# Kernel optimization log

Hardware: AMD Instinct MI355X
Metric: run time of the kernel (lower is better)

The kernel has to match this reference:

```python
import jax, jax.numpy as jnp
import numpy as np

N_GROUP = 8
TOPK_GROUP = 4
TOP_K = 8
ROUTED_SCALING = 2.5
NUM_EXPERTS = 256
HIDDEN = 7168
TOKENS = 8192


def setup_inputs() -> dict:
    key = jax.random.key(0)
    k1, k2, k3 = jax.random.split(key, 3)
    hidden_states = jax.random.normal(k1, (TOKENS, HIDDEN), dtype=jnp.float32)
    weight = jax.random.normal(k2, (NUM_EXPERTS, HIDDEN), dtype=jnp.float32) * 0.02
    e_score_correction_bias = jax.random.normal(k3, (NUM_EXPERTS,), dtype=jnp.float32) * 0.1
    return {"hidden_states": hidden_states, "weight": weight,
            "e_score_correction_bias": e_score_correction_bias}


def reference(hidden_states, weight, e_score_correction_bias):
    # logits = x @ W^T  (fp32 gate GEMM)
    logits = jnp.einsum('th,eh->te', hidden_states.astype(jnp.float32), weight)
    scores = jax.nn.sigmoid(logits)                       # [T, E]
    swb = scores + e_score_correction_bias                # [T, E]
    T, E = swb.shape
    gsize = E // N_GROUP
    # per-group score = sum of top-2 biased scores within each group
    grouped = swb.reshape(T, N_GROUP, gsize)
    top2, _ = jax.lax.top_k(grouped, 2)                   # [T, G, 2]
    group_scores = top2.sum(axis=-1)                      # [T, G]
    # keep topk_group groups
    _, gidx = jax.lax.top_k(group_scores, TOPK_GROUP)     # [T, topk_group]
    rows = jnp.arange(T)[:, None]
    group_mask = jnp.zeros((T, N_GROUP), jnp.float32).at[rows, gidx].set(1.0)
    score_mask = jnp.repeat(group_mask, gsize, axis=-1)   # [T, E]
    swb_masked = swb * score_mask
    # top_k experts among kept groups
    _, tidx = jax.lax.top_k(swb_masked, TOP_K)            # [T, top_k]
    new_mask = jnp.zeros((T, E), jnp.float32).at[rows, tidx].set(1.0)
    sel = scores * new_mask
    score_sum = sel.sum(axis=-1, keepdims=True) + 1e-20
    return sel / score_sum * ROUTED_SCALING
```

## Files before the change

### kernel.cpp

```cpp
#include <hip/hip_runtime.h>
#include <math.h>

#define TOKENS   8192
#define HIDDEN   7168
#define NEXPERT  256
#define NGROUP   8
#define TOPKG    4
#define TOPK     8
#define SCALE    2.5f

#define BM 128
#define BN 128
#define BK 32
#define KSPLIT 4
#define KPB (HIDDEN / KSPLIT)
#define NT  (KPB / BK)
#define WTILE_BYTES 32768

#define RSTR 72

typedef _Float16 half8 __attribute__((ext_vector_type(8)));
typedef _Float16 half4 __attribute__((ext_vector_type(4)));
typedef float    floatx4 __attribute__((ext_vector_type(4)));

__device__ __forceinline__ void cvt_store(_Float16* __restrict__ H,
                                          int row, int k0, float4 v) {
    half4 h, l;
    h[0] = (_Float16)v.x; h[1] = (_Float16)v.y;
    h[2] = (_Float16)v.z; h[3] = (_Float16)v.w;
    l[0] = (_Float16)(v.x - (float)h[0]);
    l[1] = (_Float16)(v.y - (float)h[1]);
    l[2] = (_Float16)(v.z - (float)h[2]);
    l[3] = (_Float16)(v.w - (float)h[3]);
    const int base = row * RSTR + ((k0 >> 3) << 4) + (k0 & 7);
    *(half4*)&H[base]     = h;
    *(half4*)&H[base + 8] = l;
}

__device__ __forceinline__ void cvt8(const float4 a, const float4 b,
                                     half8& h, half8& l) {
    h[0] = (_Float16)a.x; h[1] = (_Float16)a.y;
    h[2] = (_Float16)a.z; h[3] = (_Float16)a.w;
    h[4] = (_Float16)b.x; h[5] = (_Float16)b.y;
    h[6] = (_Float16)b.z; h[7] = (_Float16)b.w;
    l[0] = (_Float16)(a.x - (float)h[0]); l[1] = (_Float16)(a.y - (float)h[1]);
    l[2] = (_Float16)(a.z - (float)h[2]); l[3] = (_Float16)(a.w - (float)h[3]);
    l[4] = (_Float16)(b.x - (float)h[4]); l[5] = (_Float16)(b.y - (float)h[5]);
    l[6] = (_Float16)(b.z - (float)h[6]); l[7] = (_Float16)(b.w - (float)h[7]);
}

__global__ __launch_bounds__(896) void wsplit_kernel(
    const float* __restrict__ W, char* __restrict__ WS, float* __restrict__ O)
{
    const int gt = blockIdx.x * 896 + threadIdx.x;
#pragma unroll
    for (int i = 0; i < 3; i++) {
        const int idx = gt + i * (NEXPERT * 896);
        if (idx < TOKENS * NEXPERT / 4)
            *(float4*)&O[(size_t)idx * 4] = float4{0.f, 0.f, 0.f, 0.f};
    }

    const int e  = blockIdx.x;
    const int og = threadIdx.x;
    const float4 a = *(const float4*)&W[(size_t)e * HIDDEN + og * 8];
    const float4 b = *(const float4*)&W[(size_t)e * HIDDEN + og * 8 + 4];
    half8 h, l;
    cvt8(a, b, h, l);

    const int kz = og / (KPB / 8);
    const int tt = (og % (KPB / 8)) >> 2;
    const int oc = og & 3;
    char* p = WS + (size_t)(kz * NT + tt) * WTILE_BYTES + (e * 4 + oc) * 32;
    *(half8*)p        = h;
    *(half8*)(p + 16) = l;
}

__global__ __launch_bounds__(256, 2) void gate_gemm_kernel(
    const float* __restrict__ X, const char* __restrict__ WS,
    float* __restrict__ OUT)
{
    __shared__ _Float16 Ab[2][BM * RSTR];

    const int tid = threadIdx.x;
    const int nb  = blockIdx.x * BN;
    const int mb  = blockIdx.y * BM;
    const int kb  = blockIdx.z * KPB;

    const int srow = tid >> 3;
    const int sk0  = (tid & 7) * 4;
    const float* Aptr = X + (size_t)(mb + srow) * HIDDEN + kb + sk0;

    const int lane = tid & 63, wave = tid >> 6;
    const int wm = (wave >> 1) * 64, wn = (wave & 1) * 64;
    const int fr = lane & 15, quad = lane >> 4;

    const char* Bbase = WS + (size_t)(blockIdx.z * NT) * WTILE_BYTES
                      + (nb + wn + fr) * 128 + quad * 32;

    float4 av[4];
#pragma unroll
    for (int q = 0; q < 4; q++)
        av[q] = *(const float4*)(Aptr + (size_t)(q * 32) * HIDDEN);
    half8 bhA[4], blA[4], bhB[4], blB[4];
#pragma unroll
    for (int j = 0; j < 4; j++) {
        bhA[j] = *(const half8*)(Bbase + j * 2048);
        blA[j] = *(const half8*)(Bbase + j * 2048 + 16);
    }

    floatx4 acc[4][4];
#pragma unroll
    for (int i = 0; i < 4; i++)
#pragma unroll
        for (int j = 0; j < 4; j++) acc[i][j] = floatx4{0.f, 0.f, 0.f, 0.f};

#define STEP(T, BHC, BLC, BHN, BLN)                                           \
    {                                                                         \
        _Pragma("unroll")                                                     \
        for (int q = 0; q < 4; q++)                                           \
            cvt_store(Ab[(T) & 1], q * 32 + srow, sk0, av[q]);                \
        const int tn = ((T) + 1 < NT) ? (T) + 1 : NT - 1;                     \
        _Pragma("unroll")                                                     \
        for (int q = 0; q < 4; q++)                                           \
            av[q] = *(const float4*)(Aptr + tn * BK                           \
                                     + (size_t)(q * 32) * HIDDEN);            \
        __syncthreads();                                                      \
        const _Float16* Ac = Ab[(T) & 1];                                     \
        half8 ah[4], al[4];                                                   \
        _Pragma("unroll")                                                     \
        for (int i = 0; i < 4; i++) {                                         \
            const int a = (wm + i * 16 + fr) * RSTR + quad * 16;              \
            ah[i] = *(const half8*)&Ac[a];                                    \
            al[i] = *(const half8*)&Ac[a + 8];                                \
        }                                                                     \
        const char* bp = Bbase + (size_t)tn * WTILE_BYTES;                    \
        _Pragma("unroll")                                                     \
        for (int j = 0; j < 4; j++) {                                         \
            BHN[j] = *(const half8*)(bp + j * 2048);                          \
            BLN[j] = *(const half8*)(bp + j * 2048 + 16);                     \
        }                                                                     \
        _Pragma("unroll")                                                     \
        for (int j = 0; j < 4; j++)                                           \
            _Pragma("unroll")                                                 \
            for (int i = 0; i < 4; i++) {                                     \
                acc[i][j] = __builtin_amdgcn_mfma_f32_16x16x32_f16(           \
                    al[i], BHC[j], acc[i][j], 0, 0, 0);                       \
                acc[i][j] = __builtin_amdgcn_mfma_f32_16x16x32_f16(           \
                    ah[i], BLC[j], acc[i][j], 0, 0, 0);                       \
                acc[i][j] = __builtin_amdgcn_mfma_f32_16x16x32_f16(           \
                    ah[i], BHC[j], acc[i][j], 0, 0, 0);                       \
            }                                                                 \
    }

    for (int t = 0; t < NT; t += 2) {
        STEP(t,     bhA, blA, bhB, blB)
        STEP(t + 1, bhB, blB, bhA, blA)
    }
#undef STEP

#pragma unroll
    for (int i = 0; i < 4; i++)
#pragma unroll
        for (int j = 0; j < 4; j++) {
            const int col = nb + wn + j * 16 + fr;
#pragma unroll
            for (int r = 0; r < 4; r++) {
                const int row = mb + wm + i * 16 + quad * 4 + r;
                atomicAdd(&OUT[(size_t)row * NEXPERT + col], acc[i][j][r]);
            }
        }
}

__global__ __launch_bounds__(256) void route_kernel(
    float* __restrict__ S, const float* __restrict__ bias)
{
    const int lane = threadIdx.x & 63;
    const int wave = threadIdx.x >> 6;
    const int t    = blockIdx.x * 4 + wave;

    const float4 lg4 = *(const float4*)&S[(size_t)t * NEXPERT + lane * 4];
    const float4 b4  = *(const float4*)&bias[lane * 4];
    float sc[4];
    sc[0] = 1.0f / (1.0f + expf(-lg4.x));
    sc[1] = 1.0f / (1.0f + expf(-lg4.y));
    sc[2] = 1.0f / (1.0f + expf(-lg4.z));
    sc[3] = 1.0f / (1.0f + expf(-lg4.w));
    float swb[4] = { sc[0] + b4.x, sc[1] + b4.y, sc[2] + b4.z, sc[3] + b4.w };

    float m1 = -INFINITY, m2 = -INFINITY;
#pragma unroll
    for (int j = 0; j < 4; j++) {
        const float v = swb[j];
        if (v > m1)      { m2 = m1; m1 = v; }
        else if (v > m2) { m2 = v; }
    }
#pragma unroll
    for (int s = 1; s < 8; s <<= 1) {
        const float o1 = __shfl_xor(m1, s, 64);
        const float o2 = __shfl_xor(m2, s, 64);
        const float hi = fmaxf(m1, o1);
        const float lo = fminf(m1, o1);
        m2 = fmaxf(lo, fmaxf(m2, o2));
        m1 = hi;
    }
    const float gs = m1 + m2;

    float gsc[NGROUP];
#pragma unroll
    for (int g = 0; g < NGROUP; g++) gsc[g] = __shfl(gs, g * 8, 64);
    const int myg = lane >> 3;
    int rank = 0;
#pragma unroll
    for (int g = 0; g < NGROUP; g++)
        rank += (gsc[g] > gs) || (gsc[g] == gs && g < myg);
    const bool kept = (rank < TOPKG);

    float v[4];
#pragma unroll
    for (int j = 0; j < 4; j++) v[j] = kept ? swb[j] : 0.0f;

    float sum = 0.0f;
    int selmask = 0;
    for (int r = 0; r < TOPK; r++) {
        float bv = -INFINITY;
        int   bi = 0x7fffffff;
#pragma unroll
        for (int j = 0; j < 4; j++) {
            const bool avail = ((selmask >> j) & 1) == 0;
            if (avail && v[j] > bv) { bv = v[j]; bi = lane * 4 + j; }
        }
#pragma unroll
        for (int s = 1; s < 64; s <<= 1) {
            const float ov = __shfl_xor(bv, s, 64);
            const int   oi = __shfl_xor(bi, s, 64);
            if (ov > bv || (ov == bv && oi < bi)) { bv = ov; bi = oi; }
        }
        const int wl = bi >> 2, wj = bi & 3;
        const float mysc = (wj == 0) ? sc[0] : (wj == 1) ? sc[1]
                         : (wj == 2) ? sc[2] : sc[3];
        sum += __shfl(mysc, wl, 64);
        if (lane == wl) selmask |= (1 << wj);
    }

    const float rcp = SCALE / (sum + 1e-20f);
    float4 o;
    o.x = (selmask & 1) ? sc[0] * rcp : 0.0f;
    o.y = (selmask & 2) ? sc[1] * rcp : 0.0f;
    o.z = (selmask & 4) ? sc[2] * rcp : 0.0f;
    o.w = (selmask & 8) ? sc[3] * rcp : 0.0f;
    *(float4*)&S[(size_t)t * NEXPERT + lane * 4] = o;
}

extern "C" void kernel_launch(void* const* d_in, const int* in_sizes, int n_in,
                              void* d_out, int out_size, void* d_ws, size_t ws_size,
                              hipStream_t stream) {
    const float* X    = (const float*)d_in[0];
    const float* W    = (const float*)d_in[1];
    const float* bias = (const float*)d_in[2];
    float* out = (float*)d_out;
    char* ws = (char*)d_ws; (void)ws_size;

    wsplit_kernel<<<NEXPERT, 896, 0, stream>>>(W, ws, out);
    dim3 ggrid(NEXPERT / BN, TOKENS / BM, KSPLIT);
    gate_gemm_kernel<<<ggrid, 256, 0, stream>>>(X, ws, out);
    route_kernel<<<TOKENS / 4, 256, 0, stream>>>(out, bias);
}
```

Measured before the change: 434.3 us.

## Stage weight tiles through LDS and interleave MFMA with next-tile staging

Weights are re-laid out per 128-expert block so each GEMM block loads its B tile cooperatively into LDS, rather than each wave reading its own fragments straight from global memory. The main loop is restructured into a software pipeline: half the MFMAs run, then the next A/B tiles are converted and stored to LDS and the tile after that is prefetched, then the remaining MFMAs run, with one barrier per step. s_setprio and a sched_barrier are added to prioritise MFMA issue. The goal is less redundant global traffic for B and better overlap of loads with compute, at the cost of more LDS use (which may limit occupancy) and more registers for the double prefetch.

```diff
diff --git a/kernel.cpp b/kernel.cpp
--- a/kernel.cpp
+++ b/kernel.cpp
@@ -15,7 +15,7 @@
 #define KSPLIT 4
 #define KPB (HIDDEN / KSPLIT)
 #define NT  (KPB / BK)
-#define WTILE_BYTES 32768
+#define TILE_BYTES 16384
 
 #define RSTR 72
 
@@ -70,7 +70,9 @@
     const int kz = og / (KPB / 8);
     const int tt = (og % (KPB / 8)) >> 2;
     const int oc = og & 3;
-    char* p = WS + (size_t)(kz * NT + tt) * WTILE_BYTES + (e * 4 + oc) * 32;
+    const int row = e & 127, nb = e >> 7;
+    char* p = WS + (size_t)((nb * KSPLIT + kz) * NT + tt) * TILE_BYTES
+            + (row * 4 + oc) * 32;
     *(half8*)p        = h;
     *(half8*)(p + 16) = l;
 }
@@ -80,6 +82,7 @@
     float* __restrict__ OUT)
 {
     __shared__ _Float16 Ab[2][BM * RSTR];
+    __shared__ _Float16 Bb[2][BN * RSTR];
 
     const int tid = threadIdx.x;
     const int nb  = blockIdx.x * BN;
@@ -90,23 +93,47 @@
     const int sk0  = (tid & 7) * 4;
     const float* Aptr = X + (size_t)(mb + srow) * HIDDEN + kb + sk0;
 
+    const char* Wimg =
+        WS + (size_t)((blockIdx.x * KSPLIT + blockIdx.z) * NT) * TILE_BYTES;
+    const int bbase[2] = { (tid >> 2) * RSTR + (tid & 3) * 16,
+                           ((tid >> 2) + 64) * RSTR + (tid & 3) * 16 };
+
     const int lane = tid & 63, wave = tid >> 6;
     const int wm = (wave >> 1) * 64, wn = (wave & 1) * 64;
     const int fr = lane & 15, quad = lane >> 4;
 
-    const char* Bbase = WS + (size_t)(blockIdx.z * NT) * WTILE_BYTES
-                      + (nb + wn + fr) * 128 + quad * 32;
-
-    float4 av[4];
+    float4 avA[4], avB[4];
+    half8  nhA[2], nlA[2], nhB[2], nlB[2];
 #pragma unroll
     for (int q = 0; q < 4; q++)
-        av[q] = *(const float4*)(Aptr + (size_t)(q * 32) * HIDDEN);
-    half8 bhA[4], blA[4], bhB[4], blB[4];
-#pragma unroll
-    for (int j = 0; j < 4; j++) {
-        bhA[j] = *(const half8*)(Bbase + j * 2048);
-        blA[j] = *(const half8*)(Bbase + j * 2048 + 16);
-    }
+        avA[q] = *(const float4*)(Aptr + (size_t)(q * 32) * HIDDEN);
+#pragma unroll
+    for (int s = 0; s < 2; s++) {
+        const char* src = Wimg + (tid + 256 * s) * 32;
+        nhA[s] = *(const half8*)src;
+        nlA[s] = *(const half8*)(src + 16);
+    }
+#pragma unroll
+    for (int q = 0; q < 4; q++)
+        cvt_store(Ab[0], q * 32 + srow, sk0, avA[q]);
+#pragma unroll
+    for (int s = 0; s < 2; s++) {
+        *(half8*)&Bb[0][bbase[s]]     = nhA[s];
+        *(half8*)&Bb[0][bbase[s] + 8] = nlA[s];
+    }
+#pragma unroll
+    for (int q = 0; q < 4; q++)
+        avB[q] = *(const float4*)(Aptr + BK + (size_t)(q * 32) * HIDDEN);
+    {
+        const char* srcT = Wimg + (size_t)1 * TILE_BYTES;
+#pragma unroll
+        for (int s = 0; s < 2; s++) {
+            const char* src = srcT + (tid + 256 * s) * 32;
+            nhB[s] = *(const half8*)src;
+            nlB[s] = *(const half8*)(src + 16);
+        }
+    }
+    __syncthreads();
 
     floatx4 acc[4][4];
 #pragma unroll
@@ -114,47 +141,80 @@
 #pragma unroll
         for (int j = 0; j < 4; j++) acc[i][j] = floatx4{0.f, 0.f, 0.f, 0.f};
 
-#define STEP(T, BHC, BLC, BHN, BLN)                                           \
+#define STEP(T, AVC, NHC, NLC, AVN, NHN, NLN)                                 \
     {                                                                         \
-        _Pragma("unroll")                                                     \
-        for (int q = 0; q < 4; q++)                                           \
-            cvt_store(Ab[(T) & 1], q * 32 + srow, sk0, av[q]);                \
-        const int tn = ((T) + 1 < NT) ? (T) + 1 : NT - 1;                     \
-        _Pragma("unroll")                                                     \
-        for (int q = 0; q < 4; q++)                                           \
-            av[q] = *(const float4*)(Aptr + tn * BK                           \
-                                     + (size_t)(q * 32) * HIDDEN);            \
-        __syncthreads();                                                      \
         const _Float16* Ac = Ab[(T) & 1];                                     \
-        half8 ah[4], al[4];                                                   \
+        const _Float16* Bc = Bb[(T) & 1];                                     \
+        half8 ah[4], al[4], bh[4], bl[4];                                     \
         _Pragma("unroll")                                                     \
         for (int i = 0; i < 4; i++) {                                         \
             const int a = (wm + i * 16 + fr) * RSTR + quad * 16;              \
             ah[i] = *(const half8*)&Ac[a];                                    \
             al[i] = *(const half8*)&Ac[a + 8];                                \
         }                                                                     \
-        const char* bp = Bbase + (size_t)tn * WTILE_BYTES;                    \
         _Pragma("unroll")                                                     \
         for (int j = 0; j < 4; j++) {                                         \
-            BHN[j] = *(const half8*)(bp + j * 2048);                          \
-            BLN[j] = *(const half8*)(bp + j * 2048 + 16);                     \
+            const int b = (wn + j * 16 + fr) * RSTR + quad * 16;              \
+            bh[j] = *(const half8*)&Bc[b];                                    \
+            bl[j] = *(const half8*)&Bc[b + 8];                                \
         }                                                                     \
+        __builtin_amdgcn_s_setprio(1);                                       \
         _Pragma("unroll")                                                     \
-        for (int j = 0; j < 4; j++)                                           \
+        for (int j = 0; j < 2; j++)                                           \
             _Pragma("unroll")                                                 \
             for (int i = 0; i < 4; i++) {                                     \
                 acc[i][j] = __builtin_amdgcn_mfma_f32_16x16x32_f16(           \
-                    al[i], BHC[j], acc[i][j], 0, 0, 0);                       \
-                acc[i][j] = __builtin_amdgcn_mfma_f32_16x16x32_f16(           \
-                    ah[i], BLC[j], acc[i][j], 0, 0, 0);                       \
-                acc[i][j] = __builtin_amdgcn_mfma_f32_16x16x32_f16(           \
-                    ah[i], BHC[j], acc[i][j], 0, 0, 0);                       \
+                    al[i], bh[j], acc[i][j], 0, 0, 0);                        \
+                acc[i][j] = __builtin_amdgcn_mfma_f32_16x16x32_f16(           \
+                    ah[i], bl[j], acc[i][j], 0, 0, 0);                        \
+                acc[i][j] = __builtin_amdgcn_mfma_f32_16x16x32_f16(           \
+                    ah[i], bh[j], acc[i][j], 0, 0, 0);                        \
             }                                                                 \
+        __builtin_amdgcn_s_setprio(0);                                       \
+        if ((T) + 1 < NT) {                                                   \
+            _Float16* An = Ab[((T) + 1) & 1];                                 \
+            _Float16* Bn = Bb[((T) + 1) & 1];                                 \
+            _Pragma("unroll")                                                 \
+            for (int q = 0; q < 4; q++)                                       \
+                cvt_store(An, q * 32 + srow, sk0, AVC[q]);                    \
+            _Pragma("unroll")                                                 \
+            for (int s = 0; s < 2; s++) {                                     \
+                *(half8*)&Bn[bbase[s]]     = NHC[s];                          \
+                *(half8*)&Bn[bbase[s] + 8] = NLC[s];                          \
+            }                                                                 \
+            const int tn = ((T) + 2 < NT) ? (T) + 2 : NT - 1;                 \
+            _Pragma("unroll")                                                 \
+            for (int q = 0; q < 4; q++)                                       \
+                AVN[q] = *(const float4*)(Aptr + tn * BK                      \
+                                          + (size_t)(q * 32) * HIDDEN);       \
+            const char* srcT = Wimg + (size_t)tn * TILE_BYTES;                \
+            _Pragma("unroll")                                                 \
+            for (int s = 0; s < 2; s++) {                                     \
+                const char* src = srcT + (tid + 256 * s) * 32;                \
+                NHN[s] = *(const half8*)src;                                  \
+                NLN[s] = *(const half8*)(src + 16);                           \
+            }                                                                 \
+        }                                                                     \
+        __builtin_amdgcn_sched_barrier(0);       \
+        __builtin_amdgcn_s_setprio(1);                                       \
+        _Pragma("unroll")                                                     \
+        for (int j = 2; j < 4; j++)                                           \
+            _Pragma("unroll")                                                 \
+            for (int i = 0; i < 4; i++) {                                     \
+                acc[i][j] = __builtin_amdgcn_mfma_f32_16x16x32_f16(           \
+                    al[i], bh[j], acc[i][j], 0, 0, 0);                        \
+                acc[i][j] = __builtin_amdgcn_mfma_f32_16x16x32_f16(           \
+                    ah[i], bl[j], acc[i][j], 0, 0, 0);                        \
+                acc[i][j] = __builtin_amdgcn_mfma_f32_16x16x32_f16(           \
+                    ah[i], bh[j], acc[i][j], 0, 0, 0);                        \
+            }                                                                 \
+        __builtin_amdgcn_s_setprio(0);                                       \
+        __syncthreads();                                                      \
     }
 
     for (int t = 0; t < NT; t += 2) {
-        STEP(t,     bhA, blA, bhB, blB)
-        STEP(t + 1, bhB, blB, bhA, blA)
+        STEP(t,     avB, nhB, nlB, avA, nhA, nlA)
+        STEP(t + 1, avA, nhA, nlA, avB, nhB, nlB)
     }
 #undef STEP
 
```

Result: faster. 385.8 us (-11.2%).
